# Performance work log

Hardware: AMD Instinct MI355X
Metric: run time of the kernel (lower is better)

The kernel has to match this reference:

```python
import jax, jax.numpy as jnp
import numpy as np

# ---- problem dims (match init_kwargs / input_specs) ----
MC = 2048        # max_concepts
D = 128          # embed_dim
B = 64           # batch
L = 16           # program length
NOBJ = 128       # objects per scene
FDIM = 512       # feature_dim
NN = MC + NOBJ   # num_nodes
TEMP = 3.0       # cosine temperature
TH = 0.8         # true_th (cosine, train==val)
POS = 10.0
NEG = -10.0
YES_IDX = 0      # protocol['concepts','yes']
NO_IDX = 1       # protocol['concepts','no']
INIT_VAR = 0.001


def setup_inputs() -> dict:
    key = jax.random.key(0)
    ks = jax.random.split(key, 6)
    scene = jax.random.normal(ks[0], (B, NOBJ, FDIM), jnp.float32)
    # program[:, :, 0] = op code in [0,7), program[:, :, 1] = argument index
    program = jax.random.randint(ks[1], (B, L, 2), 0, 7, dtype=jnp.int32)
    concept_table = jax.random.normal(ks[2], (MC, D), jnp.float32) * INIT_VAR
    relation_table = jax.random.normal(ks[3], (MC, D * D), jnp.float32) * INIT_VAR
    W_feat = jax.random.normal(ks[4], (FDIM, D), jnp.float32) * INIT_VAR
    b_feat = jax.random.normal(ks[5], (D,), jnp.float32) * INIT_VAR
    return {"scene": scene, "program": program, "concept_table": concept_table,
            "relation_table": relation_table, "W_feat": W_feat, "b_feat": b_feat}


def _cos_sim(x, y, eps=1e-8):
    # torch F.cosine_similarity semantics: clamp each norm at eps
    xn = jnp.maximum(jnp.linalg.norm(x, axis=-1), eps)
    yn = jnp.maximum(jnp.linalg.norm(y, axis=-1), eps)
    return jnp.sum(x * y, axis=-1) / (xn * yn)


def reference(scene, program, concept_table, relation_table, W_feat, b_feat):
    # feature_mlp (dim_hidden == 0 -> single Linear)
    objects = scene @ W_feat + b_feat                              # [B, NOBJ, D]
    # per-step embedded arguments
    concept_args = concept_table[program[:, :, 1]]                 # [B, L, D]
    rel_args = relation_table[program[:, :, 1]].reshape(B, L, D, D)
    node_is_concept = jnp.arange(NN) < MC                          # [NN]
    # all_nodes = concat(all_concepts, objects) per sample
    all_nodes = jnp.concatenate(
        [jnp.broadcast_to(concept_table[None], (B, MC, D)), objects], axis=1)  # [B, NN, D]

    def run_sample(nodes_i, ops_i, args_i, cargs_i, rargs_i):
        att0 = jnp.ones((NN,), jnp.float32)

        def body(att, inp):
            op, arg, cvec, rmat = inp

            def f_null(a):
                return a

            def f_sel_obj(a):  # select 'object_only': zero concept slots
                return jnp.where(node_is_concept, 0.0, a)

            def f_sel_con(a):  # select 'concept_only': zero object slots
                return jnp.where(node_is_concept, a, 0.0)

            def f_verify(a):
                sim = _cos_sim(nodes_i, cvec[None, :])             # [NN]
                return jnp.minimum(a, jax.nn.sigmoid((sim - TH) * TEMP))

            def f_choose(a):
                a = jnp.where(node_is_concept, 0.0, a)
                return a.at[arg].set(1.0)

            def f_exist(a):
                s = a.max()
                yes = s * POS
                no = POS - yes
                a = jnp.full_like(a, NEG)
                return a.at[YES_IDX].set(yes).at[NO_IDX].set(no)

            def f_transfer(a):
                gather = a @ nodes_i                               # [D]
                trans = gather @ rmat                              # [D]
                sim = _cos_sim(nodes_i, trans[None, :])            # [NN]
                return jax.nn.sigmoid((sim - TH) * TEMP) * a.max()

            new = jax.lax.switch(
                op, [f_null, f_sel_obj, f_sel_con, f_verify, f_choose,
                     f_exist, f_transfer], att)
            return new, new

        _, hist = jax.lax.scan(body, att0, (ops_i, args_i, cargs_i, rargs_i))
        return hist                                                # [L, NN]

    hist = jax.vmap(run_sample)(all_nodes, program[:, :, 0], program[:, :, 1],
                                concept_args, rel_args)            # [B, L, NN]
    attn_final = hist[:, -1, :MC]                                  # [B, MC]
    out = jax.nn.log_softmax(attn_final, axis=1)
    return out, hist
```

## Files before the change

### kernel.cpp

```cpp
#include <hip/hip_runtime.h>
#include <math.h>

#define MC   2048
#define DD   128
#define BB   64
#define LL   16
#define NOBJ 128
#define FDIM 512
#define NN   (MC + NOBJ)
#define TEMPC 3.0f
#define THC   0.8f
#define POSC  10.0f
#define NEGC  (-10.0f)
#define EPSC  1e-8f
#define NARG  8
#define NINF  (-3.402823466e38f)
#define NSCALE 256.0f

#define QB   4
#define PART (NN / QB)
#define TS   512

typedef unsigned short ushort_t;
typedef float v2f __attribute__((ext_vector_type(2)));

#if defined(__has_builtin)
#if __has_builtin(__builtin_amdgcn_cvt_pk_f32_fp8)
#define HAS_HW_FP8 1
#endif
#endif

__device__ __forceinline__ float e4m3_dec1(unsigned int bv) {
    unsigned int s = (bv >> 7) & 1u, E = (bv >> 3) & 15u, M = bv & 7u;
    float v;
    if (E) v = __uint_as_float(((E + 120u) << 23) | (M << 20));
    else   v = (float)M * 0.001953125f;
    return s ? -v : v;
}
__device__ __forceinline__ v2f f8pair_sw(unsigned int w) {
    v2f r; r[0] = e4m3_dec1(w & 0xffu); r[1] = e4m3_dec1((w >> 8) & 0xffu); return r;
}
#ifdef HAS_HW_FP8
#define F8LO(u) __builtin_amdgcn_cvt_pk_f32_fp8((u), false)
#define F8HI(u) __builtin_amdgcn_cvt_pk_f32_fp8((u), true)
#else
#define F8LO(u) f8pair_sw((u) & 0xffffu)
#define F8HI(u) f8pair_sw((u) >> 16)
#endif

__device__ __forceinline__ unsigned int f32_to_e4m3(float x) {
    float a = fabsf(x);
    unsigned int s = (__float_as_uint(x) >> 31) << 7;
    if (a == 0.0f) return s;
    if (a >= 448.0f) return s | 0x7Eu;
    int e; float m = frexpf(a, &e);
    if (e >= -5) {
        int mant = (int)rintf(m * 16.0f);
        if (mant == 16) { mant = 8; e++; if (e - 1 > 8) return s | 0x7Eu; }
        return s | ((unsigned)(e - 1 + 7) << 3) | (unsigned)(mant - 8);
    } else {
        int q = (int)rintf(a * 512.0f);
        if (q >= 8) return s | 0x08u;
        return s | (unsigned)q;
    }
}

#define DEC16(u, g) do { \
    v2f _p0 = F8LO((u).x), _p1 = F8HI((u).x), _p2 = F8LO((u).y), _p3 = F8HI((u).y); \
    v2f _p4 = F8LO((u).z), _p5 = F8HI((u).z), _p6 = F8LO((u).w), _p7 = F8HI((u).w); \
    g[0]=_p0[0]; g[1]=_p0[1]; g[2]=_p1[0];  g[3]=_p1[1]; \
    g[4]=_p2[0]; g[5]=_p2[1]; g[6]=_p3[0];  g[7]=_p3[1]; \
    g[8]=_p4[0]; g[9]=_p4[1]; g[10]=_p5[0]; g[11]=_p5[1]; \
    g[12]=_p6[0]; g[13]=_p6[1]; g[14]=_p7[0]; g[15]=_p7[1]; \
} while (0)

__global__ __launch_bounds__(256) void gemm_objects(
        const float* __restrict__ scene, const float* __restrict__ W,
        const float* __restrict__ bias, float* __restrict__ obj) {
    __shared__ float sA[64][68];
    __shared__ float sB[64][68];
    const int b  = blockIdx.y;
    const int mt = (blockIdx.x >> 1) * 64;
    const int nt = (blockIdx.x & 1) * 64;
    const int tid = threadIdx.x;
    const int tx = tid & 15, ty = tid >> 4;
    float acc[4][4] = {{0.f,0.f,0.f,0.f},{0.f,0.f,0.f,0.f},{0.f,0.f,0.f,0.f},{0.f,0.f,0.f,0.f}};
    const float* sc = scene + (size_t)b * NOBJ * FDIM;
    for (int k0 = 0; k0 < FDIM; k0 += 64) {
        {
            const int o  = tid >> 2;
            const int ks = (tid & 3) * 16;
            const float4* src = (const float4*)(sc + (size_t)(mt + o) * FDIM + k0 + ks);
            #pragma unroll
            for (int j4 = 0; j4 < 4; j4++) {
                float4 v = src[j4];
                sA[ks + j4*4 + 0][o] = v.x;
                sA[ks + j4*4 + 1][o] = v.y;
                sA[ks + j4*4 + 2][o] = v.z;
                sA[ks + j4*4 + 3][o] = v.w;
            }
        }
        {
            const int kk = tid >> 2;
            const int dq = (tid & 3) * 16;
            const float4* src = (const float4*)(W + (size_t)(k0 + kk) * DD + nt + dq);
            float4* dst = (float4*)&sB[kk][dq];
            #pragma unroll
            for (int j4 = 0; j4 < 4; j4++) dst[j4] = src[j4];
        }
        __syncthreads();
        #pragma unroll 8
        for (int kk = 0; kk < 64; kk++) {
            float4 a4 = *(const float4*)&sA[kk][ty * 4];
            float4 b4 = *(const float4*)&sB[kk][tx * 4];
            float av[4] = {a4.x, a4.y, a4.z, a4.w};
            float bv[4] = {b4.x, b4.y, b4.z, b4.w};
            #pragma unroll
            for (int i = 0; i < 4; i++)
                #pragma unroll
                for (int j = 0; j < 4; j++)
                    acc[i][j] = fmaf(av[i], bv[j], acc[i][j]);
        }
        __syncthreads();
    }
    #pragma unroll
    for (int i = 0; i < 4; i++) {
        const int o = mt + ty * 4 + i;
        float4 r;
        r.x = acc[i][0] + bias[nt + tx*4 + 0];
        r.y = acc[i][1] + bias[nt + tx*4 + 1];
        r.z = acc[i][2] + bias[nt + tx*4 + 2];
        r.w = acc[i][3] + bias[nt + tx*4 + 3];
        *(float4*)(obj + ((size_t)b * NOBJ + o) * DD + nt + tx*4) = r;
    }
}

#define NBN ((MC + BB * NOBJ) / 4)

__global__ __launch_bounds__(256) void prep_fused(
        const float* __restrict__ ct, const float* __restrict__ obj,
        float* __restrict__ cnorm, float* __restrict__ onorm,
        unsigned char* __restrict__ ctf8, unsigned char* __restrict__ objf8,
        unsigned int* __restrict__ ctr,
        float* __restrict__ sigc, float* __restrict__ sigo) {
    if (blockIdx.x < NBN) {
        if (blockIdx.x == 0) {
            for (int i = threadIdx.x; i < BB * 16; i += 256) ctr[i] = 0u;
        }
        const int wid = threadIdx.x >> 6, lane = threadIdx.x & 63;
        const int r = blockIdx.x * 4 + wid;
        const float* row = (r < MC) ? (ct + (size_t)r * DD) : (obj + (size_t)(r - MC) * DD);
        unsigned char* brow = (r < MC) ? (ctf8 + (size_t)r * DD) : (objf8 + (size_t)(r - MC) * DD);
        float2 xy = *(const float2*)(row + lane * 2);
        float ss = xy.x * xy.x + xy.y * xy.y;
        #pragma unroll
        for (int off = 32; off; off >>= 1) ss += __shfl_xor(ss, off, 64);
        float nrm = fmaxf(sqrtf(ss), EPSC);
        float inv = NSCALE / nrm;
        unsigned int b0 = f32_to_e4m3(xy.x * inv);
        unsigned int b1 = f32_to_e4m3(xy.y * inv);
        *(ushort_t*)(brow + lane * 2) = (ushort_t)(b0 | (b1 << 8));
        if (lane == 0) {
            if (r < MC) cnorm[r] = nrm;
            else        onorm[r - MC] = nrm;
        }
        return;
    }
    __shared__ float cv[NARG][DD];
    __shared__ float cn[NARG];
    const int tid = threadIdx.x;
    for (int a = 0; a < NARG; a++)
        for (int i = tid; i < DD; i += 256) cv[a][i] = ct[(size_t)a * DD + i];
    __syncthreads();
    if (tid < NARG) {
        float ss = 0.f;
        for (int i = 0; i < DD; i++) ss = fmaf(cv[tid][i], cv[tid][i], ss);
        cn[tid] = fmaxf(sqrtf(ss), EPSC);
    }
    __syncthreads();
    const int sub = tid & 7, slot = tid >> 3;
    #pragma unroll
    for (int p = 0; p < 2; p++) {
        const int r = (blockIdx.x - NBN) * 64 + p * 32 + slot;
        const float* row = (r < MC) ? (ct + (size_t)r * DD) : (obj + (size_t)(r - MC) * DD);
        float4 r0 = *(const float4*)(row + sub * 16 + 0);
        float4 r1 = *(const float4*)(row + sub * 16 + 4);
        float4 r2 = *(const float4*)(row + sub * 16 + 8);
        float4 r3 = *(const float4*)(row + sub * 16 + 12);
        float ssr = 0.f;
        ssr = fmaf(r0.x, r0.x, ssr); ssr = fmaf(r0.y, r0.y, ssr);
        ssr = fmaf(r0.z, r0.z, ssr); ssr = fmaf(r0.w, r0.w, ssr);
        ssr = fmaf(r1.x, r1.x, ssr); ssr = fmaf(r1.y, r1.y, ssr);
        ssr = fmaf(r1.z, r1.z, ssr); ssr = fmaf(r1.w, r1.w, ssr);
        ssr = fmaf(r2.x, r2.x, ssr); ssr = fmaf(r2.y, r2.y, ssr);
        ssr = fmaf(r2.z, r2.z, ssr); ssr = fmaf(r2.w, r2.w, ssr);
        ssr = fmaf(r3.x, r3.x, ssr); ssr = fmaf(r3.y, r3.y, ssr);
        ssr = fmaf(r3.z, r3.z, ssr); ssr = fmaf(r3.w, r3.w, ssr);
        ssr += __shfl_xor(ssr, 1, 64);
        ssr += __shfl_xor(ssr, 2, 64);
        ssr += __shfl_xor(ssr, 4, 64);
        float rn = fmaxf(sqrtf(ssr), EPSC);
        for (int a = 0; a < NARG; a++) {
            const float* c = &cv[a][sub * 16];
            float dp = 0.f;
            dp = fmaf(r0.x, c[0], dp);  dp = fmaf(r0.y, c[1], dp);
            dp = fmaf(r0.z, c[2], dp);  dp = fmaf(r0.w, c[3], dp);
            dp = fmaf(r1.x, c[4], dp);  dp = fmaf(r1.y, c[5], dp);
            dp = fmaf(r1.z, c[6], dp);  dp = fmaf(r1.w, c[7], dp);
            dp = fmaf(r2.x, c[8], dp);  dp = fmaf(r2.y, c[9], dp);
            dp = fmaf(r2.z, c[10], dp); dp = fmaf(r2.w, c[11], dp);
            dp = fmaf(r3.x, c[12], dp); dp = fmaf(r3.y, c[13], dp);
            dp = fmaf(r3.z, c[14], dp); dp = fmaf(r3.w, c[15], dp);
            dp += __shfl_xor(dp, 1, 64);
            dp += __shfl_xor(dp, 2, 64);
            dp += __shfl_xor(dp, 4, 64);
            if (sub == 0) {
                float sim = dp / (rn * cn[a]);
                float g = 1.f / (1.f + __expf(-(sim - THC) * TEMPC));
                if (r < MC) sigc[(size_t)a * MC + r] = g;
                else {
                    int ro = r - MC, bb = ro >> 7, oo = ro & 127;
                    sigo[((size_t)bb * NARG + a) * NOBJ + oo] = g;
                }
            }
        }
    }
}


#define GATH_ROW(row_) do { \
    const int _r = (row_); \
    uint4 _u = *(const uint4*)&nd[_r * DD + ((sub ^ (_r & 7)) << 4)]; \
    const float _a = att[_r] * nrmL[_r]; \
    float _g[16]; DEC16(_u, _g); \
    _Pragma("unroll") \
    for (int _j = 0; _j < 16; _j++) ac[_j] = fmaf(_a, _g[_j], ac[_j]); \
} while (0)

#define SIM_ROW(row_, COMB) do { \
    const int _r = (row_); \
    uint4 _u = *(const uint4*)&nd[_r * DD + ((sub ^ (_r & 7)) << 4)]; \
    float _g[16]; DEC16(_u, _g); \
    float _dp = 0.f; \
    _Pragma("unroll") \
    for (int _j = 0; _j < 16; _j++) _dp = fmaf(_g[_j], vv[_j], _dp); \
    _dp += __shfl_xor(_dp, 1, 64); \
    _dp += __shfl_xor(_dp, 2, 64); \
    _dp += __shfl_xor(_dp, 4, 64); \
    if (sub == 0) { \
        const float _sim = _dp * invden; \
        const float sg = 1.f / (1.f + __expf(-(_sim - THC) * TEMPC)); \
        COMB; \
    } \
} while (0)

#define AST(p, v) __hip_atomic_store((p), (v), __ATOMIC_RELAXED, __HIP_MEMORY_SCOPE_AGENT)
#define ALD(p)    __hip_atomic_load((p), __ATOMIC_RELAXED, __HIP_MEMORY_SCOPE_AGENT)

#define QBARRIER() do { \
    __syncthreads(); \
    if (tid == 0) { \
        __hip_atomic_fetch_add(myctr, 1u, __ATOMIC_RELAXED, __HIP_MEMORY_SCOPE_AGENT); \
        const unsigned _tgt = (unsigned)(QB * epoch); \
        while (__hip_atomic_load(myctr, __ATOMIC_RELAXED, __HIP_MEMORY_SCOPE_AGENT) < _tgt) \
            __builtin_amdgcn_s_sleep(1); \
    } \
    __syncthreads(); \
} while (0)

__global__ __launch_bounds__(TS) void scan_exec(
        const float* __restrict__ ct, const float* __restrict__ rt,
        const int* __restrict__ program,
        const float* __restrict__ cnorm, const float* __restrict__ onorm,
        const float* __restrict__ sigc, const float* __restrict__ sigo,
        const unsigned char* __restrict__ ctf8, const unsigned char* __restrict__ objf8,
        float* __restrict__ gpart, unsigned int* __restrict__ ctr,
        float* __restrict__ out, float* __restrict__ hist) {

    const int b    = blockIdx.x & (BB - 1);
    const int q    = blockIdx.x >> 6;
    const int base = q * PART;
    const int tid  = threadIdx.x;
    const int lane = tid & 63, wid = tid >> 6;
    const int rg   = tid >> 3, sub = tid & 7;

    __shared__ __align__(16) unsigned char nd[PART * DD];
    __shared__ __align__(16) float att[PART];
    __shared__ __align__(16) float nrmL[PART];
    __shared__ __align__(16) float vec[DD];
    __shared__ __align__(16) float gvf[DD];
    __shared__ __align__(16) float part[14 * DD];
    __shared__ float wred[8];
    __shared__ float red2[8];
    __shared__ float s_sh;
    __shared__ float s_sh2;
    __shared__ int   sprog[2 * LL];

    const unsigned char* myobjf8 = objf8 + (size_t)b * NOBJ * DD;

    for (int idx = tid; idx < PART * 8; idx += TS) {
        const int row = idx >> 3, j = idx & 7;
        const int g   = base + row;
        const unsigned char* src = (g < MC) ? (ctf8 + (size_t)g * DD)
                                            : (myobjf8 + (size_t)(g - MC) * DD);
        uint4 v = *(const uint4*)(src + j * 16);
        *(uint4*)&nd[row * DD + ((j ^ (row & 7)) << 4)] = v;
    }
    for (int i = tid; i < PART; i += TS) {
        const int g = base + i;
        att[i]  = 1.0f;
        nrmL[i] = (g < MC) ? cnorm[g] : onorm[b * NOBJ + (g - MC)];
    }
    if (tid < 2 * LL) sprog[tid] = program[b * 2 * LL + tid];
    __syncthreads();

    unsigned int epoch = 0;
    float* gpb = gpart + (size_t)b * (2 * QB * 132);
    unsigned int* myctr = ctr + b * 16;

    for (int step = 0; step < LL; step++) {
        const int op  = sprog[2 * step];
        const int arg = sprog[2 * step + 1];
        float* hrow = hist + ((size_t)b * LL + step) * NN;

        if (op == 0) {
            for (int i = tid; i < PART; i += TS) hrow[base + i] = att[i];
        } else if (op == 1) {
            for (int i = tid; i < PART; i += TS) {
                const int g = base + i;
                const float nv = (g < MC) ? 0.0f : att[i];
                att[i] = nv; hrow[g] = nv;
            }
        } else if (op == 2) {
            for (int i = tid; i < PART; i += TS) {
                const int g = base + i;
                const float nv = (g < MC) ? att[i] : 0.0f;
                att[i] = nv; hrow[g] = nv;
            }
        } else if (op == 3 && arg < NARG) {
            const float* sc = sigc + (size_t)arg * MC;
            const float* so = sigo + ((size_t)b * NARG + arg) * NOBJ;
            for (int i = tid; i < PART; i += TS) {
                const int g = base + i;
                const float gg = (g < MC) ? sc[g] : so[g - MC];
                const float nv = fminf(att[i], gg);
                att[i] = nv; hrow[g] = nv;
            }
        } else if (op == 3) {
            __syncthreads();
            if (tid < DD) vec[tid] = ct[(size_t)arg * DD + tid];
            __syncthreads();
            const float cn = fmaxf(cnorm[arg], EPSC);
            const float invden = 1.0f / (NSCALE * cn);
            float vv[16];
            {
                const float4 v0 = *(const float4*)&vec[sub * 16 + 0];
                const float4 v1 = *(const float4*)&vec[sub * 16 + 4];
                const float4 v2 = *(const float4*)&vec[sub * 16 + 8];
                const float4 v3 = *(const float4*)&vec[sub * 16 + 12];
                vv[0]=v0.x; vv[1]=v0.y; vv[2]=v0.z; vv[3]=v0.w;
                vv[4]=v1.x; vv[5]=v1.y; vv[6]=v1.z; vv[7]=v1.w;
                vv[8]=v2.x; vv[9]=v2.y; vv[10]=v2.z; vv[11]=v2.w;
                vv[12]=v3.x; vv[13]=v3.y; vv[14]=v3.z; vv[15]=v3.w;
            }
            #pragma unroll
            for (int p = 0; p < 8; p++) SIM_ROW(rg + p * 64, att[_r] = fminf(att[_r], sg));
            if (rg < PART - 512) SIM_ROW(rg + 512, att[_r] = fminf(att[_r], sg));
            __syncthreads();
            for (int i = tid; i < PART; i += TS) hrow[base + i] = att[i];
        } else if (op == 4) {
            for (int i = tid; i < PART; i += TS) {
                const int g = base + i;
                const float nv = (g < MC) ? ((g == arg) ? 1.0f : 0.0f) : att[i];
                att[i] = nv; hrow[g] = nv;
            }
        } else if (op == 5) {
            __syncthreads();
            float lm = NINF;
            for (int i = tid; i < PART; i += TS) lm = fmaxf(lm, att[i]);
            #pragma unroll
            for (int off = 32; off; off >>= 1) lm = fmaxf(lm, __shfl_xor(lm, off, 64));
            if (lane == 0) wred[wid] = lm;
            __syncthreads();
            epoch++;
            if (tid == 0) {
                float m = wred[0];
                #pragma unroll
                for (int w = 1; w < 8; w++) m = fmaxf(m, wred[w]);
                AST(&gpb[(size_t)((epoch & 1) * QB + q) * 132 + DD], m);
            }
            QBARRIER();
            if (tid == 0) {
                float* slotR = gpb + (size_t)((epoch & 1) * QB) * 132;
                float m = NINF;
                #pragma unroll
                for (int k = 0; k < QB; k++)
                    m = fmaxf(m, ALD(&slotR[k * 132 + DD]));
                s_sh = m;
            }
            __syncthreads();
            const float s = s_sh;
            const float yes = s * POSC, no = POSC - yes;
            for (int i = tid; i < PART; i += TS) {
                const int g = base + i;
                const float nv = (g == 0) ? yes : ((g == 1) ? no : NEGC);
                att[i] = nv; hrow[g] = nv;
            }
        } else if (op == 6) {
            __syncthreads();
            const float* rm = rt + (size_t)arg * (DD * DD);
            const int half = lane >> 5, dq = (lane & 31) * 4;
            float4 rmr[8];
            #pragma unroll
            for (int j = 0; j < 8; j++) {
                const int d = wid * 16 + half * 8 + j;
                rmr[j] = *(const float4*)(rm + (size_t)d * DD + dq);
            }
            float lm = NINF;
            for (int i = tid; i < PART; i += TS) lm = fmaxf(lm, att[i]);
            #pragma unroll
            for (int off = 32; off; off >>= 1) lm = fmaxf(lm, __shfl_xor(lm, off, 64));
            if (lane == 0) wred[wid] = lm;
            float ac[16];
            #pragma unroll
            for (int j = 0; j < 16; j++) ac[j] = 0.f;
            #pragma unroll
            for (int p = 0; p < 8; p++) GATH_ROW(rg + p * 64);
            if (rg < PART - 512) GATH_ROW(rg + 512);
            #pragma unroll
            for (int j = 0; j < 16; j++) {
                ac[j] += __shfl_xor(ac[j], 8, 64);
                ac[j] += __shfl_xor(ac[j], 16, 64);
                ac[j] += __shfl_xor(ac[j], 32, 64);
            }
            if (lane < 8) {
                float* dst = &part[wid * DD + lane * 16];
                #pragma unroll
                for (int k = 0; k < 4; k++)
                    *(float4*)(dst + k * 4) = make_float4(ac[k*4], ac[k*4+1], ac[k*4+2], ac[k*4+3]);
            }
            __syncthreads();
            epoch++;
            {
                float* slotW = gpb + (size_t)((epoch & 1) * QB + q) * 132;
                if (tid < DD) {
                    float gsum = 0.f;
                    #pragma unroll
                    for (int w = 0; w < 8; w++) gsum += part[w * DD + tid];
                    AST(&slotW[tid], gsum);
                }
                if (tid == DD) {
                    float m = wred[0];
                    #pragma unroll
                    for (int w = 1; w < 8; w++) m = fmaxf(m, wred[w]);
                    AST(&slotW[DD], m);
                }
            }
            QBARRIER();
            {
                float* slotR = gpb + (size_t)((epoch & 1) * QB) * 132;
                if (tid < DD) {
                    float gsum = 0.f;
                    #pragma unroll
                    for (int k = 0; k < QB; k++)
                        gsum += ALD(&slotR[k * 132 + tid]);
                    gvf[tid] = gsum;
                }
                if (tid == DD) {
                    float m = NINF;
                    #pragma unroll
                    for (int k = 0; k < QB; k++)
                        m = fmaxf(m, ALD(&slotR[k * 132 + DD]));
                    s_sh = m;
                }
            }
            __syncthreads();
            float qx = 0.f, qy = 0.f, qz = 0.f, qw = 0.f;
            #pragma unroll
            for (int j = 0; j < 8; j++) {
                const int d = wid * 16 + half * 8 + j;
                const float g = gvf[d];
                qx = fmaf(g, rmr[j].x, qx); qy = fmaf(g, rmr[j].y, qy);
                qz = fmaf(g, rmr[j].z, qz); qw = fmaf(g, rmr[j].w, qw);
            }
            qx += __shfl_xor(qx, 32, 64); qy += __shfl_xor(qy, 32, 64);
            qz += __shfl_xor(qz, 32, 64); qw += __shfl_xor(qw, 32, 64);
            if (lane < 32) *(float4*)&part[wid * DD + dq] = make_float4(qx, qy, qz, qw);
            __syncthreads();
            if (tid < DD) {
                float t = 0.f;
                #pragma unroll
                for (int w = 0; w < 8; w++) t += part[w * DD + tid];
                vec[tid] = t;
                float ss = t * t;
                #pragma unroll
                for (int off = 32; off; off >>= 1) ss += __shfl_xor(ss, off, 64);
                if (lane == 0) red2[wid] = ss;
            }
            __syncthreads();
            const float tn = fmaxf(sqrtf(red2[0] + red2[1]), EPSC * NSCALE);
            const float invden = 1.0f / (NSCALE * tn);
            const float s = s_sh;
            float vv[16];
            {
                const float4 v0 = *(const float4*)&vec[sub * 16 + 0];
                const float4 v1 = *(const float4*)&vec[sub * 16 + 4];
                const float4 v2 = *(const float4*)&vec[sub * 16 + 8];
                const float4 v3 = *(const float4*)&vec[sub * 16 + 12];
                vv[0]=v0.x; vv[1]=v0.y; vv[2]=v0.z; vv[3]=v0.w;
                vv[4]=v1.x; vv[5]=v1.y; vv[6]=v1.z; vv[7]=v1.w;
                vv[8]=v2.x; vv[9]=v2.y; vv[10]=v2.z; vv[11]=v2.w;
                vv[12]=v3.x; vv[13]=v3.y; vv[14]=v3.z; vv[15]=v3.w;
            }
            #pragma unroll
            for (int p = 0; p < 8; p++) SIM_ROW(rg + p * 64, att[_r] = sg * s);
            if (rg < PART - 512) SIM_ROW(rg + 512, att[_r] = sg * s);
            __syncthreads();
            for (int i = tid; i < PART; i += TS) hrow[base + i] = att[i];
        }
    }

    __syncthreads();
    const int crows = (base + PART <= MC) ? PART : (MC - base);
    {
        float lm = NINF;
        for (int i = tid; i < crows; i += TS) lm = fmaxf(lm, att[i]);
        #pragma unroll
        for (int off = 32; off; off >>= 1) lm = fmaxf(lm, __shfl_xor(lm, off, 64));
        if (lane == 0) wred[wid] = lm;
    }
    __syncthreads();
    float mloc = wred[0];
    #pragma unroll
    for (int w = 1; w < 8; w++) mloc = fmaxf(mloc, wred[w]);
    {
        float lse = 0.f;
        for (int i = tid; i < crows; i += TS) lse += expf(att[i] - mloc);
        #pragma unroll
        for (int off = 32; off; off >>= 1) lse += __shfl_xor(lse, off, 64);
        if (lane == 0) red2[wid] = lse;
    }
    __syncthreads();
    epoch++;
    if (tid == 0) {
        float sloc = 0.f;
        #pragma unroll
        for (int w = 0; w < 8; w++) sloc += red2[w];
        float* slotW = gpb + (size_t)((epoch & 1) * QB + q) * 132;
        AST(&slotW[DD], mloc);
        AST(&slotW[DD + 1], sloc);
    }
    QBARRIER();
    if (tid == 0) {
        float* slotR = gpb + (size_t)((epoch & 1) * QB) * 132;
        float mg = NINF;
        float mq[QB], sq[QB];
        #pragma unroll
        for (int k = 0; k < QB; k++) {
            mq[k] = ALD(&slotR[k * 132 + DD]);
            sq[k] = ALD(&slotR[k * 132 + DD + 1]);
            mg = fmaxf(mg, mq[k]);
        }
        float se = 0.f;
        #pragma unroll
        for (int k = 0; k < QB; k++) se += sq[k] * expf(mq[k] - mg);
        s_sh  = mg;
        s_sh2 = logf(se);
    }
    __syncthreads();
    const float mglob = s_sh, ls = s_sh2;
    for (int i = tid; i < crows; i += TS)
        out[(size_t)b * MC + base + i] = att[i] - mglob - ls;
}

extern "C" void kernel_launch(void* const* d_in, const int* in_sizes, int n_in,
                              void* d_out, int out_size, void* d_ws, size_t ws_size,
                              hipStream_t stream) {
    const float* scene = (const float*)d_in[0];
    const int*   prog  = (const int*)d_in[1];
    const float* ct    = (const float*)d_in[2];
    const float* rt    = (const float*)d_in[3];
    const float* W     = (const float*)d_in[4];
    const float* bias  = (const float*)d_in[5];

    float* out  = (float*)d_out;
    float* hist = out + (size_t)BB * MC;

    float* obj   = (float*)d_ws;
    float* cnorm = obj + (size_t)BB * NOBJ * DD;
    float* onorm = cnorm + MC;
    float* sigc  = onorm + (size_t)BB * NOBJ;
    float* sigo  = sigc + (size_t)NARG * MC;
    float* gpart = sigo + (size_t)BB * NARG * NOBJ;
    unsigned int* ctrbuf = (unsigned int*)(gpart + (size_t)BB * 2 * QB * 132);
    unsigned char* ctf8  = (unsigned char*)(ctrbuf + BB * 16);
    unsigned char* objf8 = ctf8 + (size_t)MC * DD;

    gemm_objects<<<dim3(4, BB), 256, 0, stream>>>(scene, W, bias, obj);
    prep_fused<<<dim3(NBN + (MC + BB * NOBJ) / 64), 256, 0, stream>>>(
        ct, obj, cnorm, onorm, ctf8, objf8, ctrbuf, sigc, sigo);
    scan_exec<<<dim3(BB * QB), TS, 0, stream>>>(ct, rt, prog, cnorm, onorm, sigc, sigo,
                                                ctf8, objf8, gpart, ctrbuf, out, hist);
}
```

Before: 259.5 us.

## Buffer history in LDS and replace counter barrier with per-epoch flags

Each step's attention row is now kept in a shared-memory history buffer. All 16 steps are written to global memory at the end with coalesced float4 stores, instead of scattered per-step writes that sometimes needed an extra pass. The cross-block barrier now has each block store its own per-epoch flag and poll the four flags, replacing atomic add plus sleep polling. This adds about 35KB of LDS per block, shrinks the partial-sum scratch, and limits the number of barrier epochs to NEP=32.

```diff
diff --git a/kernel.cpp b/kernel.cpp
--- a/kernel.cpp
+++ b/kernel.cpp
@@ -20,6 +20,7 @@
 #define QB   4
 #define PART (NN / QB)
 #define TS   512
+#define NEP  32
 
 typedef unsigned short ushort_t;
 typedef float v2f __attribute__((ext_vector_type(2)));
@@ -141,11 +142,11 @@
         const float* __restrict__ ct, const float* __restrict__ obj,
         float* __restrict__ cnorm, float* __restrict__ onorm,
         unsigned char* __restrict__ ctf8, unsigned char* __restrict__ objf8,
-        unsigned int* __restrict__ ctr,
+        unsigned int* __restrict__ flags,
         float* __restrict__ sigc, float* __restrict__ sigo) {
     if (blockIdx.x < NBN) {
         if (blockIdx.x == 0) {
-            for (int i = threadIdx.x; i < BB * 16; i += 256) ctr[i] = 0u;
+            for (int i = threadIdx.x; i < BB * NEP * QB; i += 256) flags[i] = 0u;
         }
         const int wid = threadIdx.x >> 6, lane = threadIdx.x & 63;
         const int r = blockIdx.x * 4 + wid;
@@ -260,10 +261,10 @@
 #define QBARRIER() do { \
     __syncthreads(); \
     if (tid == 0) { \
-        __hip_atomic_fetch_add(myctr, 1u, __ATOMIC_RELAXED, __HIP_MEMORY_SCOPE_AGENT); \
-        const unsigned _tgt = (unsigned)(QB * epoch); \
-        while (__hip_atomic_load(myctr, __ATOMIC_RELAXED, __HIP_MEMORY_SCOPE_AGENT) < _tgt) \
-            __builtin_amdgcn_s_sleep(1); \
+        unsigned int* _fl = myflag + (int)epoch * QB; \
+        AST(&_fl[q], 1u); \
+        unsigned _s; \
+        do { _s = ALD(&_fl[0]) + ALD(&_fl[1]) + ALD(&_fl[2]) + ALD(&_fl[3]); } while (_s < 4u); \
     } \
     __syncthreads(); \
 } while (0)
@@ -274,7 +275,7 @@
         const float* __restrict__ cnorm, const float* __restrict__ onorm,
         const float* __restrict__ sigc, const float* __restrict__ sigo,
         const unsigned char* __restrict__ ctf8, const unsigned char* __restrict__ objf8,
-        float* __restrict__ gpart, unsigned int* __restrict__ ctr,
+        float* __restrict__ gpart, unsigned int* __restrict__ flags,
         float* __restrict__ out, float* __restrict__ hist) {
 
     const int b    = blockIdx.x & (BB - 1);
@@ -285,11 +286,12 @@
     const int rg   = tid >> 3, sub = tid & 7;
 
     __shared__ __align__(16) unsigned char nd[PART * DD];
+    __shared__ __align__(16) float histL[LL * PART];
     __shared__ __align__(16) float att[PART];
     __shared__ __align__(16) float nrmL[PART];
     __shared__ __align__(16) float vec[DD];
     __shared__ __align__(16) float gvf[DD];
-    __shared__ __align__(16) float part[14 * DD];
+    __shared__ __align__(16) float part[8 * DD];
     __shared__ float wred[8];
     __shared__ float red2[8];
     __shared__ float s_sh;
@@ -316,26 +318,26 @@
 
     unsigned int epoch = 0;
     float* gpb = gpart + (size_t)b * (2 * QB * 132);
-    unsigned int* myctr = ctr + b * 16;
+    unsigned int* myflag = flags + b * (NEP * QB);
 
     for (int step = 0; step < LL; step++) {
         const int op  = sprog[2 * step];
         const int arg = sprog[2 * step + 1];
-        float* hrow = hist + ((size_t)b * LL + step) * NN;
+        float* hL = histL + step * PART;
 
         if (op == 0) {
-            for (int i = tid; i < PART; i += TS) hrow[base + i] = att[i];
+            for (int i = tid; i < PART; i += TS) hL[i] = att[i];
         } else if (op == 1) {
             for (int i = tid; i < PART; i += TS) {
                 const int g = base + i;
                 const float nv = (g < MC) ? 0.0f : att[i];
-                att[i] = nv; hrow[g] = nv;
+                att[i] = nv; hL[i] = nv;
             }
         } else if (op == 2) {
             for (int i = tid; i < PART; i += TS) {
                 const int g = base + i;
                 const float nv = (g < MC) ? att[i] : 0.0f;
-                att[i] = nv; hrow[g] = nv;
+                att[i] = nv; hL[i] = nv;
             }
         } else if (op == 3 && arg < NARG) {
             const float* sc = sigc + (size_t)arg * MC;
@@ -344,7 +346,7 @@
                 const int g = base + i;
                 const float gg = (g < MC) ? sc[g] : so[g - MC];
                 const float nv = fminf(att[i], gg);
-                att[i] = nv; hrow[g] = nv;
+                att[i] = nv; hL[i] = nv;
             }
         } else if (op == 3) {
             __syncthreads();
@@ -364,15 +366,16 @@
                 vv[12]=v3.x; vv[13]=v3.y; vv[14]=v3.z; vv[15]=v3.w;
             }
             #pragma unroll
-            for (int p = 0; p < 8; p++) SIM_ROW(rg + p * 64, att[_r] = fminf(att[_r], sg));
-            if (rg < PART - 512) SIM_ROW(rg + 512, att[_r] = fminf(att[_r], sg));
-            __syncthreads();
-            for (int i = tid; i < PART; i += TS) hrow[base + i] = att[i];
+            for (int p = 0; p < 8; p++)
+                SIM_ROW(rg + p * 64, { const float nv = fminf(att[_r], sg); att[_r] = nv; hL[_r] = nv; });
+            if (rg < PART - 512)
+                SIM_ROW(rg + 512, { const float nv = fminf(att[_r], sg); att[_r] = nv; hL[_r] = nv; });
+            __syncthreads();
         } else if (op == 4) {
             for (int i = tid; i < PART; i += TS) {
                 const int g = base + i;
                 const float nv = (g < MC) ? ((g == arg) ? 1.0f : 0.0f) : att[i];
-                att[i] = nv; hrow[g] = nv;
+                att[i] = nv; hL[i] = nv;
             }
         } else if (op == 5) {
             __syncthreads();
@@ -404,7 +407,7 @@
             for (int i = tid; i < PART; i += TS) {
                 const int g = base + i;
                 const float nv = (g == 0) ? yes : ((g == 1) ? no : NEGC);
-                att[i] = nv; hrow[g] = nv;
+                att[i] = nv; hL[i] = nv;
             }
         } else if (op == 6) {
             __syncthreads();
@@ -513,14 +516,25 @@
                 vv[12]=v3.x; vv[13]=v3.y; vv[14]=v3.z; vv[15]=v3.w;
             }
             #pragma unroll
-            for (int p = 0; p < 8; p++) SIM_ROW(rg + p * 64, att[_r] = sg * s);
-            if (rg < PART - 512) SIM_ROW(rg + 512, att[_r] = sg * s);
-            __syncthreads();
-            for (int i = tid; i < PART; i += TS) hrow[base + i] = att[i];
+            for (int p = 0; p < 8; p++)
+                SIM_ROW(rg + p * 64, { const float nv = sg * s; att[_r] = nv; hL[_r] = nv; });
+            if (rg < PART - 512)
+                SIM_ROW(rg + 512, { const float nv = sg * s; att[_r] = nv; hL[_r] = nv; });
+            __syncthreads();
         }
     }
 
     __syncthreads();
+    {
+        const int nf4 = PART / 4;
+        for (int idx = tid; idx < LL * nf4; idx += TS) {
+            const int step = idx / nf4;
+            const int i4   = idx - step * nf4;
+            *(float4*)(hist + ((size_t)b * LL + step) * NN + base + i4 * 4) =
+                *(const float4*)&histL[step * PART + i4 * 4];
+        }
+    }
+
     const int crows = (base + PART <= MC) ? PART : (MC - base);
     {
         float lm = NINF;
@@ -592,13 +606,13 @@
     float* sigc  = onorm + (size_t)BB * NOBJ;
     float* sigo  = sigc + (size_t)NARG * MC;
     float* gpart = sigo + (size_t)BB * NARG * NOBJ;
-    unsigned int* ctrbuf = (unsigned int*)(gpart + (size_t)BB * 2 * QB * 132);
-    unsigned char* ctf8  = (unsigned char*)(ctrbuf + BB * 16);
+    unsigned int* flagbuf = (unsigned int*)(gpart + (size_t)BB * 2 * QB * 132);
+    unsigned char* ctf8  = (unsigned char*)(flagbuf + BB * NEP * QB);
     unsigned char* objf8 = ctf8 + (size_t)MC * DD;
 
     gemm_objects<<<dim3(4, BB), 256, 0, stream>>>(scene, W, bias, obj);
     prep_fused<<<dim3(NBN + (MC + BB * NOBJ) / 64), 256, 0, stream>>>(
-        ct, obj, cnorm, onorm, ctf8, objf8, ctrbuf, sigc, sigo);
+        ct, obj, cnorm, onorm, ctf8, objf8, flagbuf, sigc, sigo);
     scan_exec<<<dim3(BB * QB), TS, 0, stream>>>(ct, rt, prog, cnorm, onorm, sigc, sigo,
-                                                ctf8, objf8, gpart, ctrbuf, out, hist);
+                                                ctf8, objf8, gpart, flagbuf, out, hist);
 }
```

Result: no change. 262.6 us (+1.2%).
